# Kernel tuning notes

Hardware: AMD Instinct MI355X
Metric: run time of the kernel (lower is better)

Reference implementation:

```python
import jax, jax.numpy as jnp
import numpy as np

L_RTN = 3  # complex taps produced by the RTN head (w_rtn3 out dim = 2*L_RTN)
EPS = 1e-12


def _to_complex(x):
    # (B, 2n) real interleaved [re0, im0, re1, im1, ...] -> (B, n) complex
    return x[:, 0::2] + 1j * x[:, 1::2]


def _to_real(xc):
    # (B, n) complex -> (B, 2n) real interleaved
    b, n = xc.shape
    return jnp.stack([xc.real, xc.imag], axis=-1).reshape(b, 2 * n)


def _complex_conv_taps(h_c, x_c):
    # per-sample causal complex FIR: out[t] = sum_l h[l] * x[t-l]
    # h_c: (B, L) complex, x_c: (B, n) complex
    n = x_c.shape[1]
    out = jnp.zeros_like(x_c)
    for l in range(h_c.shape[1]):  # L is tiny and static
        shifted = jnp.pad(x_c, ((0, 0), (l, 0)))[:, :n]
        out = out + h_c[:, l:l + 1] * shifted
    return out


def setup_inputs() -> dict:
    key = jax.random.key(0)
    ks = jax.random.split(key, 16)
    B, D_IN, H1, CH, H_RTN, H2, D_OUT = 8192, 512, 4096, 256, 1024, 4096, 512
    s = 0.02  # weight init scale
    x = jax.random.normal(ks[0], (B, D_IN), jnp.float32)
    w1 = s * jax.random.normal(ks[1], (H1, D_IN), jnp.float32)
    b1 = jnp.zeros((H1,), jnp.float32)
    w2 = s * jax.random.normal(ks[2], (CH, H1), jnp.float32)
    b2 = jnp.zeros((CH,), jnp.float32)
    w_rtn1 = s * jax.random.normal(ks[3], (H_RTN, CH), jnp.float32)
    b_rtn1 = jnp.zeros((H_RTN,), jnp.float32)
    w_rtn2 = s * jax.random.normal(ks[4], (H_RTN, H_RTN), jnp.float32)
    b_rtn2 = jnp.zeros((H_RTN,), jnp.float32)
    w_rtn3 = s * jax.random.normal(ks[5], (2 * L_RTN, H_RTN), jnp.float32)
    # bias so that RTN starts near identity tap [1, 0, 0, ...]
    b_rtn3 = jnp.zeros((2 * L_RTN,), jnp.float32).at[0].set(1.0)
    w3 = s * jax.random.normal(ks[6], (H2, CH), jnp.float32)
    b3 = jnp.zeros((H2,), jnp.float32)
    w4 = s * jax.random.normal(ks[7], (D_OUT, H2), jnp.float32)
    b4 = jnp.zeros((D_OUT,), jnp.float32)
    h = jax.random.normal(ks[8], (2,), jnp.float32)
    h = h / jnp.linalg.norm(h)  # unit-power single-tap fading channel
    noise = 0.1 * jax.random.normal(ks[9], (B, CH), jnp.float32)
    return {"x": x, "w1": w1, "b1": b1, "w2": w2, "b2": b2,
            "w_rtn1": w_rtn1, "b_rtn1": b_rtn1, "w_rtn2": w_rtn2,
            "b_rtn2": b_rtn2, "w_rtn3": w_rtn3, "b_rtn3": b_rtn3,
            "w3": w3, "b3": b3, "w4": w4, "b4": b4, "h": h, "noise": noise}


def reference(x, w1, b1, w2, b2, w_rtn1, b_rtn1, w_rtn2, b_rtn2,
              w_rtn3, b_rtn3, w3, b3, w4, b4, h, noise):
    # encoder (linear1 -> relu -> linear2)
    a = jax.nn.relu(x @ w1.T + b1)
    s = a @ w2.T + b2                      # (B, 2n) channel signal
    # power normalization: sqrt(2n) * sqrt(0.5) * s / ||s||
    scale = jnp.sqrt(s.shape[1] * 0.5)
    s = scale * s / jnp.linalg.norm(s, axis=1, keepdims=True)
    tx_c = _to_complex(s)                  # (B, n) transmitted symbols
    # single-tap complex channel
    h_c = h[0] + 1j * h[1]
    y = _to_real(h_c * tx_c) + noise       # add per-sample AWGN
    y_c = _to_complex(y)
    # LS channel estimate (1 tap): h_est = <y, x> / <x, x>
    num = jnp.sum(y_c * jnp.conj(tx_c), axis=1, keepdims=True)
    den = jnp.sum(jnp.abs(tx_c) ** 2, axis=1, keepdims=True)
    h_est = num / den                      # (B, 1)
    # zero-forcing signal estimate
    x_eq = y_c * jnp.conj(h_est) / (jnp.abs(h_est) ** 2 + EPS)
    xr = _to_real(x_eq)                    # (B, 2n)
    # RTN: predict inverse taps and apply per-sample complex conv
    g = jnp.tanh(xr @ w_rtn1.T + b_rtn1)
    g = jnp.tanh(g @ w_rtn2.T + b_rtn2)
    h_inv = g @ w_rtn3.T + b_rtn3          # (B, 2*L_RTN)
    h_inv_c = h_inv[:, 0::2] + 1j * h_inv[:, 1::2]
    xr = _to_real(_complex_conv_taps(h_inv_c, _to_complex(xr)))
    # decoder (linear3 -> relu -> linear4)
    out = jax.nn.relu(xr @ w3.T + b3)
    return out @ w4.T + b4
```

## Files before the change

### kernel.cpp

```cpp
#include <hip/hip_runtime.h>
#include <hip/hip_bf16.h>
#include <math.h>

using bf16 = __hip_bfloat16;
typedef __attribute__((ext_vector_type(8))) short short8;
typedef __attribute__((ext_vector_type(4))) float float4v;

#define BM 128
#define BN 128
#define BK 64
#define LDK 72

template <typename T> __device__ inline T cvt_out(float v);
template <> __device__ inline float cvt_out<float>(float v) { return v; }
template <> __device__ inline bf16 cvt_out<bf16>(float v) { return __float2bfloat16(v); }

__global__ __launch_bounds__(256) void cvt_f32_bf16(const float* __restrict__ in,
                                                    bf16* __restrict__ out, int n) {
    int i = (blockIdx.x * blockDim.x + threadIdx.x) * 4;
    if (i < n) {
        float4 v = *(const float4*)(in + i);
        out[i + 0] = __float2bfloat16(v.x);
        out[i + 1] = __float2bfloat16(v.y);
        out[i + 2] = __float2bfloat16(v.z);
        out[i + 3] = __float2bfloat16(v.w);
    }
}

template <int ACT, typename OutT>
__global__ __launch_bounds__(256) void gemm_bt(const bf16* __restrict__ A,
                                               const bf16* __restrict__ W,
                                               const float* __restrict__ bias,
                                               OutT* __restrict__ C,
                                               int M, int N, int K) {
    __shared__ bf16 As[BM * LDK];
    __shared__ bf16 Bs[BN * LDK];

    const int tid = threadIdx.x;
    const int bm = blockIdx.y, bn = blockIdx.x;
    const int wave = tid >> 6, lane = tid & 63;
    const int wm = (wave >> 1) * 64, wn = (wave & 1) * 64;
    const int quad = lane >> 4, lrow = lane & 15;

    float4v acc[4][4] = {};

    for (int k0 = 0; k0 < K; k0 += BK) {
        __syncthreads();
#pragma unroll
        for (int t = 0; t < 4; ++t) {
            int c = tid + t * 256;
            int row = c >> 3, col = (c & 7) * 8;
            short8 va = *(const short8*)(A + (size_t)(bm * BM + row) * K + k0 + col);
            *(short8*)(As + row * LDK + col) = va;
            short8 vb = *(const short8*)(W + (size_t)(bn * BN + row) * K + k0 + col);
            *(short8*)(Bs + row * LDK + col) = vb;
        }
        __syncthreads();
#pragma unroll
        for (int kk = 0; kk < BK; kk += 32) {
            short8 af[4], bfr[4];
#pragma unroll
            for (int i = 0; i < 4; ++i)
                af[i] = *(const short8*)(As + (wm + i * 16 + lrow) * LDK + kk + quad * 8);
#pragma unroll
            for (int j = 0; j < 4; ++j)
                bfr[j] = *(const short8*)(Bs + (wn + j * 16 + lrow) * LDK + kk + quad * 8);
#pragma unroll
            for (int i = 0; i < 4; ++i)
#pragma unroll
                for (int j = 0; j < 4; ++j)
                    acc[i][j] = __builtin_amdgcn_mfma_f32_16x16x32_bf16(af[i], bfr[j], acc[i][j], 0, 0, 0);
        }
    }

#pragma unroll
    for (int i = 0; i < 4; ++i) {
        int m0 = bm * BM + wm + i * 16 + quad * 4;
#pragma unroll
        for (int j = 0; j < 4; ++j) {
            int n = bn * BN + wn + j * 16 + lrow;
            float bv = bias[n];
#pragma unroll
            for (int r = 0; r < 4; ++r) {
                float v = acc[i][j][r] + bv;
                if (ACT == 1) v = fmaxf(v, 0.f);
                else if (ACT == 2) v = tanhf(v);
                C[(size_t)(m0 + r) * N + n] = cvt_out<OutT>(v);
            }
        }
    }
}

__global__ __launch_bounds__(64) void channel_kernel(const float* __restrict__ s,
                                                     const float* __restrict__ h,
                                                     const float* __restrict__ noise,
                                                     float* __restrict__ xr_f,
                                                     bf16* __restrict__ xr_b) {
    const int b = blockIdx.x, lane = threadIdx.x;
    const float* srow = s + (size_t)b * 256;

    float ss = 0.f;
#pragma unroll
    for (int t = 0; t < 4; ++t) {
        float v = srow[lane + 64 * t];
        ss += v * v;
    }
#pragma unroll
    for (int off = 32; off; off >>= 1) ss += __shfl_xor(ss, off);
    const float inv = sqrtf(128.0f) / sqrtf(ss);

    const float hre = h[0], him = h[1];

    float yre[2], yim[2];
    float nre = 0.f, nim = 0.f, den = 0.f;
#pragma unroll
    for (int t = 0; t < 2; ++t) {
        int c = lane + 64 * t;
        float tr = srow[2 * c] * inv, ti = srow[2 * c + 1] * inv;
        float yr = hre * tr - him * ti + noise[(size_t)b * 256 + 2 * c];
        float yi = hre * ti + him * tr + noise[(size_t)b * 256 + 2 * c + 1];
        yre[t] = yr; yim[t] = yi;
        nre += yr * tr + yi * ti;
        nim += yi * tr - yr * ti;
        den += tr * tr + ti * ti;
    }
#pragma unroll
    for (int off = 32; off; off >>= 1) {
        nre += __shfl_xor(nre, off);
        nim += __shfl_xor(nim, off);
        den += __shfl_xor(den, off);
    }
    const float her = nre / den, hei = nim / den;
    const float d2 = her * her + hei * hei + 1e-12f;

#pragma unroll
    for (int t = 0; t < 2; ++t) {
        int c = lane + 64 * t;
        float xre = (yre[t] * her + yim[t] * hei) / d2;
        float xim = (yim[t] * her - yre[t] * hei) / d2;
        xr_f[(size_t)b * 256 + 2 * c] = xre;
        xr_f[(size_t)b * 256 + 2 * c + 1] = xim;
        xr_b[(size_t)b * 256 + 2 * c] = __float2bfloat16(xre);
        xr_b[(size_t)b * 256 + 2 * c + 1] = __float2bfloat16(xim);
    }
}

__global__ __launch_bounds__(64) void rtn_taps_conv(const bf16* __restrict__ g2,
                                                    const float* __restrict__ wr3,
                                                    const float* __restrict__ br3,
                                                    const float* __restrict__ xr_f,
                                                    bf16* __restrict__ xr2) {
    const int b = blockIdx.x, lane = threadIdx.x;
    const bf16* grow = g2 + (size_t)b * 1024;

    float acc[6] = {0.f, 0.f, 0.f, 0.f, 0.f, 0.f};
#pragma unroll
    for (int t = 0; t < 16; ++t) {
        int k = lane + 64 * t;
        float gv = __bfloat162float(grow[k]);
#pragma unroll
        for (int j = 0; j < 6; ++j) acc[j] += gv * wr3[j * 1024 + k];
    }
#pragma unroll
    for (int j = 0; j < 6; ++j)
#pragma unroll
        for (int off = 32; off; off >>= 1) acc[j] += __shfl_xor(acc[j], off);

    float tre[3], tim[3];
#pragma unroll
    for (int l = 0; l < 3; ++l) {
        tre[l] = acc[2 * l] + br3[2 * l];
        tim[l] = acc[2 * l + 1] + br3[2 * l + 1];
    }

    const float* xrow = xr_f + (size_t)b * 256;
#pragma unroll
    for (int t = 0; t < 2; ++t) {
        int c = lane + 64 * t;
        float ore = 0.f, oim = 0.f;
#pragma unroll
        for (int l = 0; l < 3; ++l) {
            int cc = c - l;
            if (cc >= 0) {
                float xre = xrow[2 * cc], xim = xrow[2 * cc + 1];
                ore += tre[l] * xre - tim[l] * xim;
                oim += tre[l] * xim + tim[l] * xre;
            }
        }
        xr2[(size_t)b * 256 + 2 * c] = __float2bfloat16(ore);
        xr2[(size_t)b * 256 + 2 * c + 1] = __float2bfloat16(oim);
    }
}

extern "C" void kernel_launch(void* const* d_in, const int* in_sizes, int n_in,
                              void* d_out, int out_size, void* d_ws, size_t ws_size,
                              hipStream_t stream) {
    constexpr int B = 8192, D_IN = 512, H1 = 4096, CH = 256, HR = 1024, H2 = 4096, DOUT = 512;

    const float* x   = (const float*)d_in[0];
    const float* w1  = (const float*)d_in[1];
    const float* b1  = (const float*)d_in[2];
    const float* w2  = (const float*)d_in[3];
    const float* b2  = (const float*)d_in[4];
    const float* wr1 = (const float*)d_in[5];
    const float* br1 = (const float*)d_in[6];
    const float* wr2 = (const float*)d_in[7];
    const float* br2 = (const float*)d_in[8];
    const float* wr3 = (const float*)d_in[9];
    const float* br3 = (const float*)d_in[10];
    const float* w3  = (const float*)d_in[11];
    const float* b3  = (const float*)d_in[12];
    const float* w4  = (const float*)d_in[13];
    const float* b4  = (const float*)d_in[14];
    const float* h   = (const float*)d_in[15];
    const float* noise = (const float*)d_in[16];

    char* ws = (char*)d_ws;
    bf16*  a    = (bf16*)(ws + 0);
    bf16*  g1   = (bf16*)(ws + 0);
    bf16*  g2   = (bf16*)(ws + 16777216);
    bf16*  tbuf = (bf16*)(ws + 0);
    bf16*  xB   = (bf16*)(ws + 67108864);
    float* sF   = (float*)(ws + 75497472);
    float* xrF  = (float*)(ws + 83886080);
    bf16*  xrB  = (bf16*)(ws + 92274688);
    bf16*  xr2  = (bf16*)(ws + 96468992);
    bf16*  w1B  = (bf16*)(ws + 100663296);
    bf16*  w2B  = (bf16*)(ws + 104857600);
    bf16*  wr1B = (bf16*)(ws + 106954752);
    bf16*  wr2B = (bf16*)(ws + 107479040);
    bf16*  w3B  = (bf16*)(ws + 109576192);
    bf16*  w4B  = (bf16*)(ws + 111673344);

    dim3 blk(256);

    auto cvt = [&](const float* src, bf16* dst, int n) {
        cvt_f32_bf16<<<(n / 4 + 255) / 256, blk, 0, stream>>>(src, dst, n);
    };
    cvt(x,   xB,   B * D_IN);
    cvt(w1,  w1B,  H1 * D_IN);
    cvt(w2,  w2B,  CH * H1);
    cvt(wr1, wr1B, HR * CH);
    cvt(wr2, wr2B, HR * HR);
    cvt(w3,  w3B,  H2 * CH);
    cvt(w4,  w4B,  DOUT * H2);

    gemm_bt<1, bf16><<<dim3(H1 / BN, B / BM), blk, 0, stream>>>(xB, w1B, b1, a, B, H1, D_IN);
    gemm_bt<0, float><<<dim3(CH / BN, B / BM), blk, 0, stream>>>(a, w2B, b2, sF, B, CH, H1);
    channel_kernel<<<B, 64, 0, stream>>>(sF, h, noise, xrF, xrB);
    gemm_bt<2, bf16><<<dim3(HR / BN, B / BM), blk, 0, stream>>>(xrB, wr1B, br1, g1, B, HR, CH);
    gemm_bt<2, bf16><<<dim3(HR / BN, B / BM), blk, 0, stream>>>(g1, wr2B, br2, g2, B, HR, HR);
    rtn_taps_conv<<<B, 64, 0, stream>>>(g2, wr3, br3, xrF, xr2);
    gemm_bt<1, bf16><<<dim3(H2 / BN, B / BM), blk, 0, stream>>>(xr2, w3B, b3, tbuf, B, H2, CH);
    gemm_bt<0, float><<<dim3(DOUT / BN, B / BM), blk, 0, stream>>>(tbuf, w4B, b4, (float*)d_out, B, DOUT, H2);
}
```

Before: 426.9 us.

## Split-K with atomics for narrow GEMMs and direct global-to-LDS loads

Adds a split-K grid dimension with float atomic accumulation for the two GEMMs with small N and large K, pre-filling outputs with bias, so the under-occupied launches use more CUs. Also replaces register-staged tile loads with global_load_lds direct-to-LDS transfers and drops the LDS row padding. The unpadded layout risks LDS bank conflicts on fragment reads, and atomics add nondeterminism and extra memory traffic.

```diff
diff --git a/kernel.cpp b/kernel.cpp
--- a/kernel.cpp
+++ b/kernel.cpp
@@ -9,11 +9,16 @@
 #define BM 128
 #define BN 128
 #define BK 64
-#define LDK 72
 
 template <typename T> __device__ inline T cvt_out(float v);
 template <> __device__ inline float cvt_out<float>(float v) { return v; }
 template <> __device__ inline bf16 cvt_out<bf16>(float v) { return __float2bfloat16(v); }
+
+__device__ inline void gload_lds16(const bf16* g, bf16* l) {
+    __builtin_amdgcn_global_load_lds(
+        (const __attribute__((address_space(1))) void*)g,
+        (__attribute__((address_space(3))) void*)l, 16, 0, 0);
+}
 
 __global__ __launch_bounds__(256) void cvt_f32_bf16(const float* __restrict__ in,
                                                     bf16* __restrict__ out, int n) {
@@ -27,33 +32,46 @@
     }
 }
 
-template <int ACT, typename OutT>
+__global__ __launch_bounds__(256) void fill_bias(float* __restrict__ out,
+                                                 const float* __restrict__ bias,
+                                                 int nmask, int total4) {
+    int i = blockIdx.x * blockDim.x + threadIdx.x;
+    if (i < total4) {
+        int idx = i * 4;
+        *(float4*)(out + idx) = *(const float4*)(bias + (idx & nmask));
+    }
+}
+
+template <int ACT, typename OutT, bool ATOMIC>
 __global__ __launch_bounds__(256) void gemm_bt(const bf16* __restrict__ A,
                                                const bf16* __restrict__ W,
                                                const float* __restrict__ bias,
                                                OutT* __restrict__ C,
-                                               int M, int N, int K) {
-    __shared__ bf16 As[BM * LDK];
-    __shared__ bf16 Bs[BN * LDK];
+                                               int M, int N, int K, int Kc) {
+    __shared__ bf16 As[BM * BK];
+    __shared__ bf16 Bs[BN * BK];
 
     const int tid = threadIdx.x;
     const int bm = blockIdx.y, bn = blockIdx.x;
     const int wave = tid >> 6, lane = tid & 63;
     const int wm = (wave >> 1) * 64, wn = (wave & 1) * 64;
     const int quad = lane >> 4, lrow = lane & 15;
+    const int kbeg = blockIdx.z * Kc;
+
+    const int chunk_base[4] = {wave * 64, 256 + wave * 64, 512 + wave * 64, 768 + wave * 64};
 
     float4v acc[4][4] = {};
-
-    for (int k0 = 0; k0 < K; k0 += BK) {
+    const size_t arow = (size_t)(bm * BM) * K;
+    const size_t brow = (size_t)(bn * BN) * K;
+
+    for (int k0 = kbeg; k0 < kbeg + Kc; k0 += BK) {
         __syncthreads();
 #pragma unroll
         for (int t = 0; t < 4; ++t) {
-            int c = tid + t * 256;
-            int row = c >> 3, col = (c & 7) * 8;
-            short8 va = *(const short8*)(A + (size_t)(bm * BM + row) * K + k0 + col);
-            *(short8*)(As + row * LDK + col) = va;
-            short8 vb = *(const short8*)(W + (size_t)(bn * BN + row) * K + k0 + col);
-            *(short8*)(Bs + row * LDK + col) = vb;
+            int chunk = chunk_base[t] + lane;
+            int row = chunk >> 3, col = (chunk & 7) * 8;
+            gload_lds16(A + arow + (size_t)row * K + k0 + col, As + chunk_base[t] * 8);
+            gload_lds16(W + brow + (size_t)row * K + k0 + col, Bs + chunk_base[t] * 8);
         }
         __syncthreads();
 #pragma unroll
@@ -61,10 +79,10 @@
             short8 af[4], bfr[4];
 #pragma unroll
             for (int i = 0; i < 4; ++i)
-                af[i] = *(const short8*)(As + (wm + i * 16 + lrow) * LDK + kk + quad * 8);
+                af[i] = *(const short8*)(As + (wm + i * 16 + lrow) * BK + kk + quad * 8);
 #pragma unroll
             for (int j = 0; j < 4; ++j)
-                bfr[j] = *(const short8*)(Bs + (wn + j * 16 + lrow) * LDK + kk + quad * 8);
+                bfr[j] = *(const short8*)(Bs + (wn + j * 16 + lrow) * BK + kk + quad * 8);
 #pragma unroll
             for (int i = 0; i < 4; ++i)
 #pragma unroll
@@ -79,13 +97,19 @@
 #pragma unroll
         for (int j = 0; j < 4; ++j) {
             int n = bn * BN + wn + j * 16 + lrow;
-            float bv = bias[n];
-#pragma unroll
-            for (int r = 0; r < 4; ++r) {
-                float v = acc[i][j][r] + bv;
-                if (ACT == 1) v = fmaxf(v, 0.f);
-                else if (ACT == 2) v = tanhf(v);
-                C[(size_t)(m0 + r) * N + n] = cvt_out<OutT>(v);
+            if constexpr (ATOMIC) {
+#pragma unroll
+                for (int r = 0; r < 4; ++r)
+                    atomicAdd((float*)&C[(size_t)(m0 + r) * N + n], acc[i][j][r]);
+            } else {
+                float bv = bias[n];
+#pragma unroll
+                for (int r = 0; r < 4; ++r) {
+                    float v = acc[i][j][r] + bv;
+                    if (ACT == 1) v = fmaxf(v, 0.f);
+                    else if (ACT == 2) v = tanhf(v);
+                    C[(size_t)(m0 + r) * N + n] = cvt_out<OutT>(v);
+                }
             }
         }
     }
@@ -245,12 +269,21 @@
     cvt(w3,  w3B,  H2 * CH);
     cvt(w4,  w4B,  DOUT * H2);
 
-    gemm_bt<1, bf16><<<dim3(H1 / BN, B / BM), blk, 0, stream>>>(xB, w1B, b1, a, B, H1, D_IN);
-    gemm_bt<0, float><<<dim3(CH / BN, B / BM), blk, 0, stream>>>(a, w2B, b2, sF, B, CH, H1);
+    gemm_bt<1, bf16, false><<<dim3(H1 / BN, B / BM, 1), blk, 0, stream>>>(
+        xB, w1B, b1, a, B, H1, D_IN, D_IN);
+    fill_bias<<<(B * CH / 4 + 255) / 256, blk, 0, stream>>>(sF, b2, CH - 1, B * CH / 4);
+    gemm_bt<0, float, true><<<dim3(CH / BN, B / BM, 8), blk, 0, stream>>>(
+        a, w2B, nullptr, sF, B, CH, H1, H1 / 8);
     channel_kernel<<<B, 64, 0, stream>>>(sF, h, noise, xrF, xrB);
-    gemm_bt<2, bf16><<<dim3(HR / BN, B / BM), blk, 0, stream>>>(xrB, wr1B, br1, g1, B, HR, CH);
-    gemm_bt<2, bf16><<<dim3(HR / BN, B / BM), blk, 0, stream>>>(g1, wr2B, br2, g2, B, HR, HR);
+    gemm_bt<2, bf16, false><<<dim3(HR / BN, B / BM, 1), blk, 0, stream>>>(
+        xrB, wr1B, br1, g1, B, HR, CH, CH);
+    gemm_bt<2, bf16, false><<<dim3(HR / BN, B / BM, 1), blk, 0, stream>>>(
+        g1, wr2B, br2, g2, B, HR, HR, HR);
     rtn_taps_conv<<<B, 64, 0, stream>>>(g2, wr3, br3, xrF, xr2);
-    gemm_bt<1, bf16><<<dim3(H2 / BN, B / BM), blk, 0, stream>>>(xr2, w3B, b3, tbuf, B, H2, CH);
-    gemm_bt<0, float><<<dim3(DOUT / BN, B / BM), blk, 0, stream>>>(tbuf, w4B, b4, (float*)d_out, B, DOUT, H2);
-}
+    gemm_bt<1, bf16, false><<<dim3(H2 / BN, B / BM, 1), blk, 0, stream>>>(
+        xr2, w3B, b3, tbuf, B, H2, CH, CH);
+    fill_bias<<<(B * DOUT / 4 + 255) / 256, blk, 0, stream>>>(
+        (float*)d_out, b4, DOUT - 1, B * DOUT / 4);
+    gemm_bt<0, float, true><<<dim3(DOUT / BN, B / BM, 4), blk, 0, stream>>>(
+        tbuf, w4B, nullptr, (float*)d_out, B, DOUT, H2, H2 / 4);
+}
```

Measured after the change: 483.3 us. 1.13x slower.

## Use direct global-to-LDS loads, per-GEMM tile shapes, and one fused conversion kernel

Applied to the files above, without the earlier changes.

Stage GEMM tiles with the global_load_lds builtin, which writes straight into shared memory without passing through registers. The GEMM kernel is templated on wave tile counts and BK, so each layer gets its own tile shape, with smaller tiles for the narrow-N GEMMs (N=256 and N=512) to launch more workgroups. The seven separate fp32-to-bf16 conversion launches become one packed launch. As a trade-off, the LDS layout loses its padding (row stride now equals BK), which may cause bank conflicts on the fragment reads.

```diff
diff --git a/kernel.cpp b/kernel.cpp
--- a/kernel.cpp
+++ b/kernel.cpp
@@ -6,79 +6,106 @@
 typedef __attribute__((ext_vector_type(8))) short short8;
 typedef __attribute__((ext_vector_type(4))) float float4v;
 
-#define BM 128
-#define BN 128
-#define BK 64
-#define LDK 72
-
 template <typename T> __device__ inline T cvt_out(float v);
 template <> __device__ inline float cvt_out<float>(float v) { return v; }
 template <> __device__ inline bf16 cvt_out<bf16>(float v) { return __float2bfloat16(v); }
 
-__global__ __launch_bounds__(256) void cvt_f32_bf16(const float* __restrict__ in,
-                                                    bf16* __restrict__ out, int n) {
-    int i = (blockIdx.x * blockDim.x + threadIdx.x) * 4;
-    if (i < n) {
-        float4 v = *(const float4*)(in + i);
-        out[i + 0] = __float2bfloat16(v.x);
-        out[i + 1] = __float2bfloat16(v.y);
-        out[i + 2] = __float2bfloat16(v.z);
-        out[i + 3] = __float2bfloat16(v.w);
-    }
-}
-
-template <int ACT, typename OutT>
+__device__ inline void gload_lds16(const bf16* g, bf16* l) {
+    __builtin_amdgcn_global_load_lds(
+        (const __attribute__((address_space(1))) void*)g,
+        (__attribute__((address_space(3))) void*)l, 16, 0, 0);
+}
+
+struct CvtPack {
+    const float* src[7];
+    bf16* dst[7];
+    int end[7];
+};
+
+__global__ __launch_bounds__(256) void cvt_all(CvtPack p) {
+    int e = (blockIdx.x * 256 + threadIdx.x) * 4;
+    int start = 0;
+#pragma unroll
+    for (int s = 0; s < 7; ++s) {
+        if (e < p.end[s]) {
+            int off = e - start;
+            float4 v = *(const float4*)(p.src[s] + off);
+            bf16* d = p.dst[s] + off;
+            d[0] = __float2bfloat16(v.x);
+            d[1] = __float2bfloat16(v.y);
+            d[2] = __float2bfloat16(v.z);
+            d[3] = __float2bfloat16(v.w);
+            return;
+        }
+        start = p.end[s];
+    }
+}
+
+template <int ACT, typename OutT, int WMT, int WNT, int BKT>
 __global__ __launch_bounds__(256) void gemm_bt(const bf16* __restrict__ A,
                                                const bf16* __restrict__ W,
                                                const float* __restrict__ bias,
                                                OutT* __restrict__ C,
                                                int M, int N, int K) {
-    __shared__ bf16 As[BM * LDK];
-    __shared__ bf16 Bs[BN * LDK];
+    constexpr int TBM = 32 * WMT;
+    constexpr int TBN = 32 * WNT;
+    constexpr int CPR = BKT / 8;
+    constexpr int CA = TBM * CPR;
+    constexpr int CB = TBN * CPR;
+
+    __shared__ bf16 As[TBM * BKT];
+    __shared__ bf16 Bs[TBN * BKT];
 
     const int tid = threadIdx.x;
     const int bm = blockIdx.y, bn = blockIdx.x;
     const int wave = tid >> 6, lane = tid & 63;
-    const int wm = (wave >> 1) * 64, wn = (wave & 1) * 64;
+    const int wm = (wave >> 1) * (16 * WMT), wn = (wave & 1) * (16 * WNT);
     const int quad = lane >> 4, lrow = lane & 15;
 
-    float4v acc[4][4] = {};
-
-    for (int k0 = 0; k0 < K; k0 += BK) {
+    float4v acc[WMT][WNT] = {};
+    const size_t arow = (size_t)(bm * TBM) * K;
+    const size_t brow = (size_t)(bn * TBN) * K;
+
+    for (int k0 = 0; k0 < K; k0 += BKT) {
         __syncthreads();
 #pragma unroll
-        for (int t = 0; t < 4; ++t) {
-            int c = tid + t * 256;
-            int row = c >> 3, col = (c & 7) * 8;
-            short8 va = *(const short8*)(A + (size_t)(bm * BM + row) * K + k0 + col);
-            *(short8*)(As + row * LDK + col) = va;
-            short8 vb = *(const short8*)(W + (size_t)(bn * BN + row) * K + k0 + col);
-            *(short8*)(Bs + row * LDK + col) = vb;
+        for (int t = 0; t < CA / 256; ++t) {
+            int base = t * 256 + wave * 64;
+            int c = base + lane;
+            int row = c / CPR, col = (c % CPR) * 8;
+            gload_lds16(A + arow + (size_t)row * K + k0 + col, As + base * 8);
+        }
+#pragma unroll
+        for (int t = 0; t < CB / 256; ++t) {
+            int base = t * 256 + wave * 64;
+            int c = base + lane;
+            int row = c / CPR, col = (c % CPR) * 8;
+            gload_lds16(W + brow + (size_t)row * K + k0 + col, Bs + base * 8);
         }
         __syncthreads();
 #pragma unroll
-        for (int kk = 0; kk < BK; kk += 32) {
-            short8 af[4], bfr[4];
-#pragma unroll
-            for (int i = 0; i < 4; ++i)
-                af[i] = *(const short8*)(As + (wm + i * 16 + lrow) * LDK + kk + quad * 8);
-#pragma unroll
-            for (int j = 0; j < 4; ++j)
-                bfr[j] = *(const short8*)(Bs + (wn + j * 16 + lrow) * LDK + kk + quad * 8);
-#pragma unroll
-            for (int i = 0; i < 4; ++i)
-#pragma unroll
-                for (int j = 0; j < 4; ++j)
+        for (int kk = 0; kk < BKT; kk += 32) {
+            short8 af[WMT], bfr[WNT];
+#pragma unroll
+            for (int i = 0; i < WMT; ++i)
+                af[i] = *(const short8*)(As + (wm + i * 16 + lrow) * BKT + kk + quad * 8);
+#pragma unroll
+            for (int j = 0; j < WNT; ++j)
+                bfr[j] = *(const short8*)(Bs + (wn + j * 16 + lrow) * BKT + kk + quad * 8);
+#pragma unroll
+            for (int i = 0; i < WMT; ++i)
+#pragma unroll
+                for (int j = 0; j < WNT; ++j)
                     acc[i][j] = __builtin_amdgcn_mfma_f32_16x16x32_bf16(af[i], bfr[j], acc[i][j], 0, 0, 0);
         }
     }
 
 #pragma unroll
-    for (int i = 0; i < 4; ++i) {
-        int m0 = bm * BM + wm + i * 16 + quad * 4;
-#pragma unroll
-        for (int j = 0; j < 4; ++j) {
-            int n = bn * BN + wn + j * 16 + lrow;
+    for (int i = 0; i < WMT; ++i) {
+        int m0 = bm * TBM + wm + i * 16 + quad * 4;
+#pragma unroll
+        for (int j = 0; j < WNT; ++j) {
+            int n = bn * TBN + wn + j * 16 + lrow;
             float bv = bias[n];
 #pragma unroll
             for (int r = 0; r < 4; ++r) {
@@ -234,23 +261,26 @@
 
     dim3 blk(256);
 
-    auto cvt = [&](const float* src, bf16* dst, int n) {
-        cvt_f32_bf16<<<(n / 4 + 255) / 256, blk, 0, stream>>>(src, dst, n);
-    };
-    cvt(x,   xB,   B * D_IN);
-    cvt(w1,  w1B,  H1 * D_IN);
-    cvt(w2,  w2B,  CH * H1);
-    cvt(wr1, wr1B, HR * CH);
-    cvt(wr2, wr2B, HR * HR);
-    cvt(w3,  w3B,  H2 * CH);
-    cvt(w4,  w4B,  DOUT * H2);
-
-    gemm_bt<1, bf16><<<dim3(H1 / BN, B / BM), blk, 0, stream>>>(xB, w1B, b1, a, B, H1, D_IN);
-    gemm_bt<0, float><<<dim3(CH / BN, B / BM), blk, 0, stream>>>(a, w2B, b2, sF, B, CH, H1);
+    CvtPack p;
+    const float* srcs[7] = {x, w1, w2, wr1, wr2, w3, w4};
+    bf16* dsts[7] = {xB, w1B, w2B, wr1B, wr2B, w3B, w4B};
+    int ns[7] = {B * D_IN, H1 * D_IN, CH * H1, HR * CH, HR * HR, H2 * CH, DOUT * H2};
+    int cum = 0;
+    for (int i = 0; i < 7; ++i) { p.src[i] = srcs[i]; p.dst[i] = dsts[i]; cum += ns[i]; p.end[i] = cum; }
+    cvt_all<<<(cum / 4 + 255) / 256, blk, 0, stream>>>(p);
+
+    gemm_bt<1, bf16, 4, 4, 64><<<dim3(H1 / 128, B / 128), blk, 0, stream>>>(
+        xB, w1B, b1, a, B, H1, D_IN);
+    gemm_bt<0, float, 2, 2, 128><<<dim3(CH / 64, B / 64), blk, 0, stream>>>(
+        a, w2B, b2, sF, B, CH, H1);
     channel_kernel<<<B, 64, 0, stream>>>(sF, h, noise, xrF, xrB);
-    gemm_bt<2, bf16><<<dim3(HR / BN, B / BM), blk, 0, stream>>>(xrB, wr1B, br1, g1, B, HR, CH);
-    gemm_bt<2, bf16><<<dim3(HR / BN, B / BM), blk, 0, stream>>>(g1, wr2B, br2, g2, B, HR, HR);
+    gemm_bt<2, bf16, 4, 2, 64><<<dim3(HR / 64, B / 128), blk, 0, stream>>>(
+        xrB, wr1B, br1, g1, B, HR, CH);
+    gemm_bt<2, bf16, 4, 2, 64><<<dim3(HR / 64, B / 128), blk, 0, stream>>>(
+        g1, wr2B, br2, g2, B, HR, HR);
     rtn_taps_conv<<<B, 64, 0, stream>>>(g2, wr3, br3, xrF, xr2);
-    gemm_bt<1, bf16><<<dim3(H2 / BN, B / BM), blk, 0, stream>>>(xr2, w3B, b3, tbuf, B, H2, CH);
-    gemm_bt<0, float><<<dim3(DOUT / BN, B / BM), blk, 0, stream>>>(tbuf, w4B, b4, (float*)d_out, B, DOUT, H2);
-}
+    gemm_bt<1, bf16, 4, 4, 64><<<dim3(H2 / 128, B / 128), blk, 0, stream>>>(
+        xr2, w3B, b3, tbuf, B, H2, CH);
+    gemm_bt<0, float, 4, 2, 128><<<dim3(DOUT / 64, B / 128), blk, 0, stream>>>(
+        tbuf, w4B, b4, (float*)d_out, B, DOUT, H2);
+}
```

New measurement: 442.1 us. +3.6%, slower.
